# Performance work log

Hardware: AMD Instinct MI355X
Metric: run time of the kernel (lower is better)

The kernel has to match this reference:

```python
import jax, jax.numpy as jnp
import numpy as np

NUM_STEPS = 100
FRACTAL_STEPS = 1


def setup_inputs() -> dict:
    key = jax.random.key(0)
    B, D, NF = 16384, 256, 32  # batch, input_shape(==num_hidden), num_filters
    ks = jax.random.split(key, 6)

    def lin_w(k, fin, fout):
        return (jax.random.normal(k, (fin, fout), jnp.float32) / np.sqrt(fin)).astype(jnp.float32)

    return {
        "x": jax.random.normal(ks[0], (B, D), jnp.float32),
        "alpha": jnp.ones((D,), jnp.float32),
        "sigma": jnp.ones((D,), jnp.float32),
        "enc_w1": lin_w(ks[1], D, NF), "enc_b1": jnp.zeros((NF,), jnp.float32),
        "enc_w2": lin_w(ks[2], NF, D), "enc_b2": jnp.zeros((D,), jnp.float32),
        "gen_w1": lin_w(ks[3], D, NF), "gen_b1": jnp.zeros((NF,), jnp.float32),
        "gen_w2": lin_w(ks[4], NF, NF), "gen_b2": jnp.zeros((NF,), jnp.float32),
        "gen_w3": lin_w(ks[5], NF, D), "gen_b3": jnp.zeros((D,), jnp.float32),
    }


def reference(x, alpha, sigma, enc_w1, enc_b1, enc_w2, enc_b2,
              gen_w1, gen_b1, gen_w2, gen_b2, gen_w3, gen_b3):
    base_key = jax.random.key(42)
    D = x.shape[-1]

    def diffuse(z, i):
        # alpha_t = exp(-0.5*alpha*t/T), sigma_t = exp(0.5*sigma*t/T)
        t = i / NUM_STEPS
        a = jnp.exp(-0.5 * alpha * t)
        s = jnp.exp(0.5 * sigma * t)
        noise = jax.random.normal(jax.random.fold_in(base_key, i), z.shape, z.dtype)
        return z * a + s * noise

    # encoder: Linear -> ReLU -> Linear
    z = jnp.maximum(x @ enc_w1 + enc_b1, 0.0) @ enc_w2 + enc_b2  # [B, D]
    z = jnp.tile(z, (FRACTAL_STEPS, 1))

    def step(z, i):
        z = diffuse(z, i)
        h = jnp.maximum(z @ gen_w1 + gen_b1, 0.0)
        h = jnp.maximum(h @ gen_w2 + gen_b2, 0.0)
        z = jnp.maximum(h @ gen_w3 + gen_b3, 0.0)  # generator output then F.relu
        return z, None

    # loop i = T-1 .. 1 (diffuse + generator); the i == 0 iteration only diffuses
    ts = jnp.arange(NUM_STEPS - 1, 0, -1)
    z, _ = jax.lax.scan(step, z, ts)
    z = diffuse(z, jnp.int32(0))
    return z.reshape(-1, D)
```

## Files before the change

kernel.cpp:

```cpp
#include <hip/hip_runtime.h>
#include <stdint.h>


#define NUM_STEPS 100
#define HALFB 8192
#define THREADS 512
#define ZSTR 264
#define WS 36

#define Z_OFF   0
#define W1_OFF  (Z_OFF + 64*ZSTR)
#define W3_OFF  (W1_OFF + 256*32)
#define W2_OFF  (W3_OFF + 256*WS)
#define HB_OFF  (W2_OFF + 32*WS)
#define AE_OFF  (HB_OFF + 64*WS)
#define SE_OFF  (AE_OFF + 512)
#define B1_OFF  (SE_OFF + 512)
#define B2_OFF  (B1_OFF + 32)
#define B3_OFF  (B2_OFF + 32)
#define LDS_FLOATS (B3_OFF + 256)
#define LDS_BYTES  (LDS_FLOATS * 4)

static_assert(LDS_BYTES <= 160*1024, "LDS overflow");

typedef float v2f __attribute__((ext_vector_type(2)));
typedef float v4f __attribute__((ext_vector_type(4)));

#define PKFMA(acc,s0,s1)   asm("v_pk_fma_f32 %0, %1, %2, %0" : "+v"(acc) : "v"(s0), "v"(s1))
#define PKFMA_L(acc,s0,s1) asm("v_pk_fma_f32 %0, %1, %2, %0 op_sel:[0,0,0] op_sel_hi:[0,1,1]" : "+v"(acc) : "v"(s0), "v"(s1))
#define PKFMA_H(acc,s0,s1) asm("v_pk_fma_f32 %0, %1, %2, %0 op_sel:[1,0,0] op_sel_hi:[1,1,1]" : "+v"(acc) : "v"(s0), "v"(s1))
#define PKMUL(d,a,b)       asm("v_pk_mul_f32 %0, %1, %2" : "=v"(d) : "v"(a), "v"(b))

__device__ __forceinline__ uint32_t rotl32(uint32_t v, int n) {
  return (v << n) | (v >> (32 - n));
}

__device__ __forceinline__ void tf2x32(uint32_t k0, uint32_t k1,
                                       uint32_t& x0, uint32_t& x1) {
  uint32_t k2 = k0 ^ k1 ^ 0x1BD11BDAu;
  x0 += k0; x1 += k1;
#define TFR(r) { x0 += x1; x1 = rotl32(x1,(r)); x1 ^= x0; }
  TFR(13) TFR(15) TFR(26) TFR(6)
  x0 += k1; x1 += k2 + 1u;
  TFR(17) TFR(29) TFR(16) TFR(24)
  x0 += k2; x1 += k0 + 2u;
  TFR(13) TFR(15) TFR(26) TFR(6)
  x0 += k0; x1 += k1 + 3u;
  TFR(17) TFR(29) TFR(16) TFR(24)
  x0 += k1; x1 += k2 + 4u;
  TFR(13) TFR(15) TFR(26) TFR(6)
  x0 += k2; x1 += k0 + 5u;
#undef TFR
}

__device__ __forceinline__ uint32_t tf_bits(uint32_t k0, uint32_t k1, uint32_t n) {
  uint32_t x0 = 0u, x1 = n;
  tf2x32(k0, k1, x0, x1);
  return x0 ^ x1;
}

__device__ __forceinline__ v2f b2n_pk(uint32_t b0, uint32_t b1) {
  const float MN = -0.99999994039535522461f;
  v2f f = { __uint_as_float((b0 >> 9) | 0x3F800000u),
            __uint_as_float((b1 >> 9) | 0x3F800000u) };
  v2f fm = f - 1.0f;
  v2f u = __builtin_elementwise_fma(fm, (v2f)2.0f, (v2f)MN);
  u = __builtin_elementwise_max(u, (v2f)MN);
  v2f x2 = u * u;
  v2f om = 1.0f - x2;
  v2f w  = { -__logf(om.x), -__logf(om.y) };
  v2f ws = w - 2.5f;
  v2f ps = (v2f)2.81022636e-08f;
  ps = __builtin_elementwise_fma(ps, ws, (v2f)3.43273939e-07f);
  ps = __builtin_elementwise_fma(ps, ws, (v2f)-3.5233877e-06f);
  ps = __builtin_elementwise_fma(ps, ws, (v2f)-4.39150654e-06f);
  ps = __builtin_elementwise_fma(ps, ws, (v2f)0.00021858087f);
  ps = __builtin_elementwise_fma(ps, ws, (v2f)-0.00125372503f);
  ps = __builtin_elementwise_fma(ps, ws, (v2f)-0.00417768164f);
  ps = __builtin_elementwise_fma(ps, ws, (v2f)0.246640727f);
  ps = __builtin_elementwise_fma(ps, ws, (v2f)1.50140941f);
  v2f sq = { sqrtf(w.x), sqrtf(w.y) };
  v2f wb = sq - 3.0f;
  v2f pb = (v2f)-0.000200214257f;
  pb = __builtin_elementwise_fma(pb, wb, (v2f)0.000100950558f);
  pb = __builtin_elementwise_fma(pb, wb, (v2f)0.00134934322f);
  pb = __builtin_elementwise_fma(pb, wb, (v2f)-0.00367342844f);
  pb = __builtin_elementwise_fma(pb, wb, (v2f)0.00573950773f);
  pb = __builtin_elementwise_fma(pb, wb, (v2f)-0.0076224613f);
  pb = __builtin_elementwise_fma(pb, wb, (v2f)0.00943887047f);
  pb = __builtin_elementwise_fma(pb, wb, (v2f)1.00167406f);
  pb = __builtin_elementwise_fma(pb, wb, (v2f)2.83297682f);
  v2f p = { (w.x < 5.0f) ? ps.x : pb.x,
            (w.y < 5.0f) ? ps.y : pb.y };
  return (p * u) * 1.41421356237309515f;
}

__global__ __launch_bounds__(THREADS, 2)
void gdiff_kernel(const float* __restrict__ x,
                  const float* __restrict__ alpha, const float* __restrict__ sigma,
                  const float* __restrict__ ew1, const float* __restrict__ eb1,
                  const float* __restrict__ ew2, const float* __restrict__ eb2,
                  const float* __restrict__ gw1, const float* __restrict__ gb1,
                  const float* __restrict__ gw2, const float* __restrict__ gb2,
                  const float* __restrict__ gw3, const float* __restrict__ gb3,
                  float* __restrict__ out)
{
  extern __shared__ float sm[];
  const int t    = threadIdx.x;
  const int pr   = t >> 4;
  const int c    = t & 15;
  const int half = c >> 3;
  const int cf   = c & 7;
  const int rid  = pr + (half << 5);
  const int zrow = rid * ZSTR;
  const uint32_t rowg = (uint32_t)(blockIdx.x * 32 + pr) + (uint32_t)(half * HALFB);
  const uint32_t nb   = rowg * 256u + (uint32_t)cf;

  v4f hq0, hq1, hq2, hq3, hq4, hq5, hq6, hq7;

  auto stage_w1 = [&](const float* __restrict__ w) {
    const int r = t >> 1, hh = t & 1;
#pragma unroll
    for (int q = 0; q < 4; ++q)
      *(v4f*)&sm[W1_OFF + r * 32 + hh * 16 + 4 * q] =
          *(const v4f*)&w[r * 32 + hh * 16 + 4 * q];
  };
  auto stage_w3t = [&](const float* __restrict__ w) {
    const int g = t >> 4, dc = t & 15;
#pragma unroll
    for (int q = 0; q < 4; ++q) {
      const int d0 = dc * 16 + q * 4;
      v4f v = *(const v4f*)&w[g * 256 + d0];
      sm[W3_OFF + (d0 + 0) * WS + g] = v.x;
      sm[W3_OFF + (d0 + 1) * WS + g] = v.y;
      sm[W3_OFF + (d0 + 2) * WS + g] = v.z;
      sm[W3_OFF + (d0 + 3) * WS + g] = v.w;
    }
  };

  auto layer1 = [&](v2f& h01, v2f& h23) {
    v4f bv = *(const v4f*)&sm[B1_OFF + 4 * cf];
    h01 = bv.xy; h23 = bv.zw;
    const float* zr_ = &sm[Z_OFF + zrow];
    const float* wp  = &sm[W1_OFF + 4 * cf];
#pragma unroll 4
    for (int d0 = 0; d0 < 256; d0 += 4) {
      v4f z4 = *(const v4f*)&zr_[d0];
      v4f wa = *(const v4f*)&wp[(d0 + 0) * 32];
      v4f wb = *(const v4f*)&wp[(d0 + 1) * 32];
      v4f wc = *(const v4f*)&wp[(d0 + 2) * 32];
      v4f wd = *(const v4f*)&wp[(d0 + 3) * 32];
      PKFMA_L(h01, z4.xy, wa.xy); PKFMA_L(h23, z4.xy, wa.zw);
      PKFMA_H(h01, z4.xy, wb.xy); PKFMA_H(h23, z4.xy, wb.zw);
      PKFMA_L(h01, z4.zw, wc.xy); PKFMA_L(h23, z4.zw, wc.zw);
      PKFMA_H(h01, z4.zw, wd.xy); PKFMA_H(h23, z4.zw, wd.zw);
    }
  };
  auto hwrite = [&](v2f a, v2f b) {
    v4f hv; hv.xy = a; hv.zw = b;
    *(v4f*)&sm[HB_OFF + rid * WS + 4 * cf] = hv;
  };
  auto hload = [&]() {
    const float* hb = &sm[HB_OFF + rid * WS];
    hq0 = *(const v4f*)&hb[0];  hq1 = *(const v4f*)&hb[4];
    hq2 = *(const v4f*)&hb[8];  hq3 = *(const v4f*)&hb[12];
    hq4 = *(const v4f*)&hb[16]; hq5 = *(const v4f*)&hb[20];
    hq6 = *(const v4f*)&hb[24]; hq7 = *(const v4f*)&hb[28];
  };
  auto layer2 = [&](v2f& g01, v2f& g23) {
    v4f bv = *(const v4f*)&sm[B2_OFF + 4 * cf];
    g01 = bv.xy; g23 = bv.zw;
    const float* w2c = &sm[W2_OFF + 4 * cf];
#define L2M(hq, m) { \
    v4f wA = *(const v4f*)&w2c[(4*(m)+0)*WS]; \
    v4f wB = *(const v4f*)&w2c[(4*(m)+1)*WS]; \
    v4f wC = *(const v4f*)&w2c[(4*(m)+2)*WS]; \
    v4f wD = *(const v4f*)&w2c[(4*(m)+3)*WS]; \
    PKFMA_L(g01, hq.xy, wA.xy); PKFMA_L(g23, hq.xy, wA.zw); \
    PKFMA_H(g01, hq.xy, wB.xy); PKFMA_H(g23, hq.xy, wB.zw); \
    PKFMA_L(g01, hq.zw, wC.xy); PKFMA_L(g23, hq.zw, wC.zw); \
    PKFMA_H(g01, hq.zw, wD.xy); PKFMA_H(g23, hq.zw, wD.zw); }
    L2M(hq0,0) L2M(hq1,1) L2M(hq2,2) L2M(hq3,3)
    L2M(hq4,4) L2M(hq5,5) L2M(hq6,6) L2M(hq7,7)
#undef L2M
  };
  auto l3d = [&](uint32_t c0p, uint32_t c1p, const float* ae, const float* se, bool relu) {
    const float* w3b = &sm[W3_OFF];
#pragma unroll 2
    for (int kp = 0; kp < 16; ++kp) {
      const int dlo = cf + 16 * kp;
      const int dhi = dlo + 8;
      v2f acc0 = { sm[B3_OFF + dlo], 0.f };
      v2f acc1 = { sm[B3_OFF + dhi], 0.f };
      const float* wl = &w3b[dlo * WS];
      const float* wh = &w3b[dhi * WS];
#define L3M(hq, off) { \
      v4f wvl = *(const v4f*)&wl[off]; \
      v4f wvh = *(const v4f*)&wh[off]; \
      PKFMA(acc0, hq.xy, wvl.xy); PKFMA(acc0, hq.zw, wvl.zw); \
      PKFMA(acc1, hq.xy, wvh.xy); PKFMA(acc1, hq.zw, wvh.zw); }
      L3M(hq0, 0)  L3M(hq1, 4)  L3M(hq2, 8)  L3M(hq3, 12)
      L3M(hq4, 16) L3M(hq5, 20) L3M(hq6, 24) L3M(hq7, 28)
#undef L3M
      float z0 = acc0.x + acc0.y;
      float z1 = acc1.x + acc1.y;
      if (relu) { z0 = fmaxf(z0, 0.f); z1 = fmaxf(z1, 0.f); }
      const uint32_t n0 = nb + (uint32_t)(16 * kp);
      const uint32_t b0 = tf_bits(c0p, c1p, n0);
      const uint32_t b1 = tf_bits(c0p, c1p, n0 + 8u);
      v2f nrm = b2n_pk(b0, b1);
      v2f a2 = { ae[dlo], ae[dhi] };
      v2f s2 = { se[dlo], se[dhi] };
      v2f z2 = { z0, z1 };
      v2f zd; PKMUL(zd, z2, a2); PKFMA(zd, s2, nrm);
      sm[Z_OFF + zrow + dlo] = zd.x;
      sm[Z_OFF + zrow + dhi] = zd.y;
    }
  };

  {
    const int zr = t >> 3, jj = t & 7;
    const int gr = (zr < 32) ? (blockIdx.x * 32 + zr)
                             : (blockIdx.x * 32 + zr - 32 + HALFB);
    const v4f* src = (const v4f*)(x + (size_t)gr * 256 + jj * 32);
#pragma unroll
    for (int q = 0; q < 8; ++q)
      *(v4f*)&sm[Z_OFF + zr * ZSTR + jj * 32 + q * 4] = src[q];
  }
  stage_w1(ew1);
  stage_w3t(ew2);
  if (t < 256) sm[B3_OFF + t] = eb2[t];
  if (t < 32)  sm[B1_OFF + t] = eb1[t];
  {
    const float t99 = 99.0f / 100.0f;
    if (t < 256) sm[AE_OFF + 256 + t]       = __expf(-0.5f * alpha[t] * t99);
    else         sm[SE_OFF + 256 + (t-256)] = __expf( 0.5f * sigma[t-256] * t99);
  }
  __syncthreads();

  {
    v2f h01, h23;
    layer1(h01, h23);
    h01 = __builtin_elementwise_max(h01, (v2f)0.f);
    h23 = __builtin_elementwise_max(h23, (v2f)0.f);
    hwrite(h01, h23);
    hload();
    uint32_t e0 = 0u, e1 = 99u;
    tf2x32(0u, 42u, e0, e1);
    l3d(e0, e1, &sm[AE_OFF + 256], &sm[SE_OFF + 256], false);
  }
  __syncthreads();

  stage_w1(gw1);
  stage_w3t(gw3);
  if (t < 256) {
    sm[B3_OFF + t] = gb3[t];
    if (t < 32) { sm[B1_OFF + t] = gb1[t]; sm[B2_OFF + t] = gb2[t]; }
    const int r = t >> 3, s8 = t & 7;
    *(v4f*)&sm[W2_OFF + r * WS + 4 * s8] = *(const v4f*)&gw2[r * 32 + 4 * s8];
  }
  __syncthreads();

#pragma unroll 1
  for (int i = 99; i >= 1; --i) {
    const int j = i - 1;
    const float tt = (float)j / 100.0f;
    const int buf = (j & 1) << 8;
    if (t < 256) sm[AE_OFF + buf + t]       = __expf(-0.5f * alpha[t] * tt);
    else         sm[SE_OFF + buf + (t-256)] = __expf( 0.5f * sigma[t-256] * tt);
    __syncthreads();

    v2f h01, h23;
    layer1(h01, h23);
    h01 = __builtin_elementwise_max(h01, (v2f)0.f);
    h23 = __builtin_elementwise_max(h23, (v2f)0.f);
    hwrite(h01, h23);
    hload();

    v2f g01, g23;
    layer2(g01, g23);
    g01 = __builtin_elementwise_max(g01, (v2f)0.f);
    g23 = __builtin_elementwise_max(g23, (v2f)0.f);
    hwrite(g01, g23);
    hload();

    uint32_t e0 = 0u, e1 = (uint32_t)j;
    tf2x32(0u, 42u, e0, e1);
    l3d(e0, e1, &sm[AE_OFF + buf], &sm[SE_OFF + buf], true);
  }
  __syncthreads();

  {
    const int zr = t >> 3, jj = t & 7;
    const int gr = (zr < 32) ? (blockIdx.x * 32 + zr)
                             : (blockIdx.x * 32 + zr - 32 + HALFB);
    v4f* dst = (v4f*)(out + (size_t)gr * 256 + jj * 32);
#pragma unroll
    for (int q = 0; q < 8; ++q)
      dst[q] = *(const v4f*)&sm[Z_OFF + zr * ZSTR + jj * 32 + q * 4];
  }
}

extern "C" void kernel_launch(void* const* d_in, const int* in_sizes, int n_in,
                              void* d_out, int out_size, void* d_ws, size_t ws_size,
                              hipStream_t stream) {
  (void)in_sizes; (void)n_in; (void)d_ws; (void)ws_size; (void)out_size;
  const float* x     = (const float*)d_in[0];
  const float* alpha = (const float*)d_in[1];
  const float* sigma = (const float*)d_in[2];
  const float* ew1   = (const float*)d_in[3];
  const float* eb1   = (const float*)d_in[4];
  const float* ew2   = (const float*)d_in[5];
  const float* eb2   = (const float*)d_in[6];
  const float* gw1   = (const float*)d_in[7];
  const float* gb1   = (const float*)d_in[8];
  const float* gw2   = (const float*)d_in[9];
  const float* gb2   = (const float*)d_in[10];
  const float* gw3   = (const float*)d_in[11];
  const float* gb3   = (const float*)d_in[12];
  float* out = (float*)d_out;

  (void)hipFuncSetAttribute((const void*)gdiff_kernel,
                            hipFuncAttributeMaxDynamicSharedMemorySize, LDS_BYTES);

  gdiff_kernel<<<256, THREADS, LDS_BYTES, stream>>>(
      x, alpha, sigma, ew1, eb1, ew2, eb2, gw1, gb1, gw2, gb2, gw3, gb3, out);
}
```

Baseline: 3.220 ms.

## Double threads per block with split-K layers, register diffusion coefficients, and branchy RNG

Raises the block to 1024 threads and splits the layer-1 and layer-2 reductions across two thread halves, combining them with a cross-lane shuffle. Each thread now produces 16 output columns instead of 32 in layer 3. Diffusion coefficients move into registers and are updated each step by multiplying with precomputed per-step ratios, which removes the per-step exp and one barrier. The change also uses alignbit for rotates and skips the large-tail branch of the inverse-erf polynomial unless some lane needs it. The risks are higher register pressure under the 4-wave occupancy bound, drift from the repeated coefficient multiplication, and the hoisted half-row z offset in LDS.

```diff
diff --git a/kernel.cpp b/kernel.cpp
--- a/kernel.cpp
+++ b/kernel.cpp
@@ -2,20 +2,19 @@
 #include <stdint.h>
 
 
-#define NUM_STEPS 100
 #define HALFB 8192
-#define THREADS 512
+#define THREADS 1024
 #define ZSTR 264
 #define WS 36
 
 #define Z_OFF   0
-#define W1_OFF  (Z_OFF + 64*ZSTR)
-#define W3_OFF  (W1_OFF + 256*32)
-#define W2_OFF  (W3_OFF + 256*WS)
-#define HB_OFF  (W2_OFF + 32*WS)
-#define AE_OFF  (HB_OFF + 64*WS)
-#define SE_OFF  (AE_OFF + 512)
-#define B1_OFF  (SE_OFF + 512)
+#define W1_OFF  16896
+#define W3_OFF  (W1_OFF + 8192)
+#define W2_OFF  (W3_OFF + 9216)
+#define HB_OFF  (W2_OFF + 1152)
+#define IA_OFF  (HB_OFF + 64*WS)
+#define IS_OFF  (IA_OFF + 256)
+#define B1_OFF  (IS_OFF + 256)
 #define B2_OFF  (B1_OFF + 32)
 #define B3_OFF  (B2_OFF + 32)
 #define LDS_FLOATS (B3_OFF + 256)
@@ -32,7 +31,7 @@
 #define PKMUL(d,a,b)       asm("v_pk_mul_f32 %0, %1, %2" : "=v"(d) : "v"(a), "v"(b))
 
 __device__ __forceinline__ uint32_t rotl32(uint32_t v, int n) {
-  return (v << n) | (v >> (32 - n));
+  return __builtin_amdgcn_alignbit(v, v, (uint32_t)(32 - n));
 }
 
 __device__ __forceinline__ void tf2x32(uint32_t k0, uint32_t k1,
@@ -79,23 +78,27 @@
   ps = __builtin_elementwise_fma(ps, ws, (v2f)-0.00417768164f);
   ps = __builtin_elementwise_fma(ps, ws, (v2f)0.246640727f);
   ps = __builtin_elementwise_fma(ps, ws, (v2f)1.50140941f);
-  v2f sq = { sqrtf(w.x), sqrtf(w.y) };
-  v2f wb = sq - 3.0f;
-  v2f pb = (v2f)-0.000200214257f;
-  pb = __builtin_elementwise_fma(pb, wb, (v2f)0.000100950558f);
-  pb = __builtin_elementwise_fma(pb, wb, (v2f)0.00134934322f);
-  pb = __builtin_elementwise_fma(pb, wb, (v2f)-0.00367342844f);
-  pb = __builtin_elementwise_fma(pb, wb, (v2f)0.00573950773f);
-  pb = __builtin_elementwise_fma(pb, wb, (v2f)-0.0076224613f);
-  pb = __builtin_elementwise_fma(pb, wb, (v2f)0.00943887047f);
-  pb = __builtin_elementwise_fma(pb, wb, (v2f)1.00167406f);
-  pb = __builtin_elementwise_fma(pb, wb, (v2f)2.83297682f);
-  v2f p = { (w.x < 5.0f) ? ps.x : pb.x,
-            (w.y < 5.0f) ? ps.y : pb.y };
+  v2f p = ps;
+  const int big = (w.x >= 5.0f) | (w.y >= 5.0f);
+  if (__any(big)) {
+    v2f sq = { sqrtf(w.x), sqrtf(w.y) };
+    v2f wb = sq - 3.0f;
+    v2f pb = (v2f)-0.000200214257f;
+    pb = __builtin_elementwise_fma(pb, wb, (v2f)0.000100950558f);
+    pb = __builtin_elementwise_fma(pb, wb, (v2f)0.00134934322f);
+    pb = __builtin_elementwise_fma(pb, wb, (v2f)-0.00367342844f);
+    pb = __builtin_elementwise_fma(pb, wb, (v2f)0.00573950773f);
+    pb = __builtin_elementwise_fma(pb, wb, (v2f)-0.0076224613f);
+    pb = __builtin_elementwise_fma(pb, wb, (v2f)0.00943887047f);
+    pb = __builtin_elementwise_fma(pb, wb, (v2f)1.00167406f);
+    pb = __builtin_elementwise_fma(pb, wb, (v2f)2.83297682f);
+    p.x = (w.x < 5.0f) ? ps.x : pb.x;
+    p.y = (w.y < 5.0f) ? ps.y : pb.y;
+  }
   return (p * u) * 1.41421356237309515f;
 }
 
-__global__ __launch_bounds__(THREADS, 2)
+__global__ __launch_bounds__(THREADS, 4)
 void gdiff_kernel(const float* __restrict__ x,
                   const float* __restrict__ alpha, const float* __restrict__ sigma,
                   const float* __restrict__ ew1, const float* __restrict__ eb1,
@@ -107,29 +110,32 @@
 {
   extern __shared__ float sm[];
   const int t    = threadIdx.x;
-  const int pr   = t >> 4;
-  const int c    = t & 15;
-  const int half = c >> 3;
-  const int cf   = c & 7;
+  const int pr   = t >> 5;
+  const int c    = t & 31;
+  const int half = c >> 4;
+  const int cf   = c & 15;
+  const int q    = cf & 7;
+  const int dh   = cf >> 3;
   const int rid  = pr + (half << 5);
-  const int zrow = rid * ZSTR;
-  const uint32_t rowg = (uint32_t)(blockIdx.x * 32 + pr) + (uint32_t)(half * HALFB);
+  const int zrow = rid * ZSTR + (half << 3);
+  const uint32_t rowg = (uint32_t)(blockIdx.x * 32 + pr + half * HALFB);
   const uint32_t nb   = rowg * 256u + (uint32_t)cf;
 
   v4f hq0, hq1, hq2, hq3, hq4, hq5, hq6, hq7;
+  v2f av[8], sv[8];
 
   auto stage_w1 = [&](const float* __restrict__ w) {
-    const int r = t >> 1, hh = t & 1;
-#pragma unroll
-    for (int q = 0; q < 4; ++q)
-      *(v4f*)&sm[W1_OFF + r * 32 + hh * 16 + 4 * q] =
-          *(const v4f*)&w[r * 32 + hh * 16 + 4 * q];
+    const int r = t >> 2, part = t & 3;
+#pragma unroll
+    for (int s = 0; s < 2; ++s)
+      *(v4f*)&sm[W1_OFF + r * 32 + part * 8 + 4 * s] =
+          *(const v4f*)&w[r * 32 + part * 8 + 4 * s];
   };
   auto stage_w3t = [&](const float* __restrict__ w) {
-    const int g = t >> 4, dc = t & 15;
-#pragma unroll
-    for (int q = 0; q < 4; ++q) {
-      const int d0 = dc * 16 + q * 4;
+    const int g = t >> 5, dc = t & 31;
+#pragma unroll
+    for (int s = 0; s < 2; ++s) {
+      const int d0 = dc * 8 + s * 4;
       v4f v = *(const v4f*)&w[g * 256 + d0];
       sm[W3_OFF + (d0 + 0) * WS + g] = v.x;
       sm[W3_OFF + (d0 + 1) * WS + g] = v.y;
@@ -139,12 +145,13 @@
   };
 
   auto layer1 = [&](v2f& h01, v2f& h23) {
-    v4f bv = *(const v4f*)&sm[B1_OFF + 4 * cf];
+    v4f bv = { 0.f, 0.f, 0.f, 0.f };
+    if (!dh) bv = *(const v4f*)&sm[B1_OFF + 4 * q];
     h01 = bv.xy; h23 = bv.zw;
-    const float* zr_ = &sm[Z_OFF + zrow];
-    const float* wp  = &sm[W1_OFF + 4 * cf];
+    const float* zr_ = &sm[zrow + (dh << 7)];
+    const float* wp  = &sm[W1_OFF + (dh << 12) + 4 * q];
 #pragma unroll 4
-    for (int d0 = 0; d0 < 256; d0 += 4) {
+    for (int d0 = 0; d0 < 128; d0 += 4) {
       v4f z4 = *(const v4f*)&zr_[d0];
       v4f wa = *(const v4f*)&wp[(d0 + 0) * 32];
       v4f wb = *(const v4f*)&wp[(d0 + 1) * 32];
@@ -156,11 +163,17 @@
       PKFMA_H(h01, z4.zw, wd.xy); PKFMA_H(h23, z4.zw, wd.zw);
     }
   };
+  auto red8_relu = [&](v2f& a, v2f& b) {
+    a.x += __shfl_xor(a.x, 8); a.y += __shfl_xor(a.y, 8);
+    b.x += __shfl_xor(b.x, 8); b.y += __shfl_xor(b.y, 8);
+    a = __builtin_elementwise_max(a, (v2f)0.f);
+    b = __builtin_elementwise_max(b, (v2f)0.f);
+  };
   auto hwrite = [&](v2f a, v2f b) {
-    v4f hv; hv.xy = a; hv.zw = b;
-    *(v4f*)&sm[HB_OFF + rid * WS + 4 * cf] = hv;
-  };
-  auto hload = [&]() {
+    if (!dh) { v4f hv; hv.xy = a; hv.zw = b;
+               *(v4f*)&sm[HB_OFF + rid * WS + 4 * q] = hv; }
+  };
+  auto hload8 = [&]() {
     const float* hb = &sm[HB_OFF + rid * WS];
     hq0 = *(const v4f*)&hb[0];  hq1 = *(const v4f*)&hb[4];
     hq2 = *(const v4f*)&hb[8];  hq3 = *(const v4f*)&hb[12];
@@ -168,86 +181,87 @@
     hq6 = *(const v4f*)&hb[24]; hq7 = *(const v4f*)&hb[28];
   };
   auto layer2 = [&](v2f& g01, v2f& g23) {
-    v4f bv = *(const v4f*)&sm[B2_OFF + 4 * cf];
+    const float* hb = &sm[HB_OFF + rid * WS + (dh << 4)];
+    v4f hA = *(const v4f*)&hb[0], hB = *(const v4f*)&hb[4];
+    v4f hC = *(const v4f*)&hb[8], hD = *(const v4f*)&hb[12];
+    v4f bv = { 0.f, 0.f, 0.f, 0.f };
+    if (!dh) bv = *(const v4f*)&sm[B2_OFF + 4 * q];
     g01 = bv.xy; g23 = bv.zw;
-    const float* w2c = &sm[W2_OFF + 4 * cf];
-#define L2M(hq, m) { \
-    v4f wA = *(const v4f*)&w2c[(4*(m)+0)*WS]; \
-    v4f wB = *(const v4f*)&w2c[(4*(m)+1)*WS]; \
-    v4f wC = *(const v4f*)&w2c[(4*(m)+2)*WS]; \
-    v4f wD = *(const v4f*)&w2c[(4*(m)+3)*WS]; \
-    PKFMA_L(g01, hq.xy, wA.xy); PKFMA_L(g23, hq.xy, wA.zw); \
-    PKFMA_H(g01, hq.xy, wB.xy); PKFMA_H(g23, hq.xy, wB.zw); \
-    PKFMA_L(g01, hq.zw, wC.xy); PKFMA_L(g23, hq.zw, wC.zw); \
-    PKFMA_H(g01, hq.zw, wD.xy); PKFMA_H(g23, hq.zw, wD.zw); }
-    L2M(hq0,0) L2M(hq1,1) L2M(hq2,2) L2M(hq3,3)
-    L2M(hq4,4) L2M(hq5,5) L2M(hq6,6) L2M(hq7,7)
+    const float* w2c = &sm[W2_OFF + (dh << 4) * WS + 4 * q];
+#define L2M(hqm, mm) { \
+    v4f wA = *(const v4f*)&w2c[(4*(mm)+0)*WS]; \
+    v4f wB = *(const v4f*)&w2c[(4*(mm)+1)*WS]; \
+    v4f wC = *(const v4f*)&w2c[(4*(mm)+2)*WS]; \
+    v4f wD = *(const v4f*)&w2c[(4*(mm)+3)*WS]; \
+    PKFMA_L(g01, hqm.xy, wA.xy); PKFMA_L(g23, hqm.xy, wA.zw); \
+    PKFMA_H(g01, hqm.xy, wB.xy); PKFMA_H(g23, hqm.xy, wB.zw); \
+    PKFMA_L(g01, hqm.zw, wC.xy); PKFMA_L(g23, hqm.zw, wC.zw); \
+    PKFMA_H(g01, hqm.zw, wD.xy); PKFMA_H(g23, hqm.zw, wD.zw); }
+    L2M(hA,0) L2M(hB,1) L2M(hC,2) L2M(hD,3)
 #undef L2M
   };
-  auto l3d = [&](uint32_t c0p, uint32_t c1p, const float* ae, const float* se, bool relu) {
-    const float* w3b = &sm[W3_OFF];
-#pragma unroll 2
-    for (int kp = 0; kp < 16; ++kp) {
-      const int dlo = cf + 16 * kp;
-      const int dhi = dlo + 8;
+  auto l3d = [&](uint32_t e0, uint32_t e1, bool relu) {
+#pragma unroll
+    for (int kp = 0; kp < 8; ++kp) {
+      const int dlo = cf + 32 * kp;
+      const int dhi = dlo + 16;
       v2f acc0 = { sm[B3_OFF + dlo], 0.f };
       v2f acc1 = { sm[B3_OFF + dhi], 0.f };
-      const float* wl = &w3b[dlo * WS];
-      const float* wh = &w3b[dhi * WS];
-#define L3M(hq, off) { \
+      const float* wl = &sm[W3_OFF + dlo * WS];
+      const float* wh = &sm[W3_OFF + dhi * WS];
+#define L3M(hqm, off) { \
       v4f wvl = *(const v4f*)&wl[off]; \
       v4f wvh = *(const v4f*)&wh[off]; \
-      PKFMA(acc0, hq.xy, wvl.xy); PKFMA(acc0, hq.zw, wvl.zw); \
-      PKFMA(acc1, hq.xy, wvh.xy); PKFMA(acc1, hq.zw, wvh.zw); }
+      PKFMA(acc0, hqm.xy, wvl.xy); PKFMA(acc0, hqm.zw, wvl.zw); \
+      PKFMA(acc1, hqm.xy, wvh.xy); PKFMA(acc1, hqm.zw, wvh.zw); }
       L3M(hq0, 0)  L3M(hq1, 4)  L3M(hq2, 8)  L3M(hq3, 12)
       L3M(hq4, 16) L3M(hq5, 20) L3M(hq6, 24) L3M(hq7, 28)
 #undef L3M
       float z0 = acc0.x + acc0.y;
       float z1 = acc1.x + acc1.y;
       if (relu) { z0 = fmaxf(z0, 0.f); z1 = fmaxf(z1, 0.f); }
-      const uint32_t n0 = nb + (uint32_t)(16 * kp);
-      const uint32_t b0 = tf_bits(c0p, c1p, n0);
-      const uint32_t b1 = tf_bits(c0p, c1p, n0 + 8u);
-      v2f nrm = b2n_pk(b0, b1);
-      v2f a2 = { ae[dlo], ae[dhi] };
-      v2f s2 = { se[dlo], se[dhi] };
+      const uint32_t n0 = nb + (uint32_t)(32 * kp);
+      v2f nrm = b2n_pk(tf_bits(e0, e1, n0), tf_bits(e0, e1, n0 + 16u));
       v2f z2 = { z0, z1 };
-      v2f zd; PKMUL(zd, z2, a2); PKFMA(zd, s2, nrm);
-      sm[Z_OFF + zrow + dlo] = zd.x;
-      sm[Z_OFF + zrow + dhi] = zd.y;
+      v2f zd; PKMUL(zd, z2, av[kp]); PKFMA(zd, sv[kp], nrm);
+      sm[zrow + dlo] = zd.x;
+      sm[zrow + dhi] = zd.y;
     }
   };
 
   {
-    const int zr = t >> 3, jj = t & 7;
+    const int zr = t >> 4, jj = t & 15;
     const int gr = (zr < 32) ? (blockIdx.x * 32 + zr)
                              : (blockIdx.x * 32 + zr - 32 + HALFB);
-    const v4f* src = (const v4f*)(x + (size_t)gr * 256 + jj * 32);
-#pragma unroll
-    for (int q = 0; q < 8; ++q)
-      *(v4f*)&sm[Z_OFF + zr * ZSTR + jj * 32 + q * 4] = src[q];
+    const v4f* src = (const v4f*)(x + (size_t)gr * 256 + jj * 16);
+    const int zb = zr * ZSTR + ((zr >> 5) << 3);
+#pragma unroll
+    for (int s = 0; s < 4; ++s)
+      *(v4f*)&sm[zb + jj * 16 + 4 * s] = src[s];
   }
   stage_w1(ew1);
   stage_w3t(ew2);
+  if (t < 256)      sm[IA_OFF + t]         = __expf( 0.5f * alpha[t] * 0.01f);
+  else if (t < 512) sm[IS_OFF + (t - 256)] = __expf(-0.5f * sigma[t - 256] * 0.01f);
   if (t < 256) sm[B3_OFF + t] = eb2[t];
   if (t < 32)  sm[B1_OFF + t] = eb1[t];
-  {
-    const float t99 = 99.0f / 100.0f;
-    if (t < 256) sm[AE_OFF + 256 + t]       = __expf(-0.5f * alpha[t] * t99);
-    else         sm[SE_OFF + 256 + (t-256)] = __expf( 0.5f * sigma[t-256] * t99);
+#pragma unroll
+  for (int kp = 0; kp < 8; ++kp) {
+    const int dlo = cf + 32 * kp, dhi = dlo + 16;
+    av[kp] = v2f{ __expf(-0.5f * alpha[dlo] * 0.99f), __expf(-0.5f * alpha[dhi] * 0.99f) };
+    sv[kp] = v2f{ __expf( 0.5f * sigma[dlo] * 0.99f), __expf( 0.5f * sigma[dhi] * 0.99f) };
   }
   __syncthreads();
 
   {
     v2f h01, h23;
     layer1(h01, h23);
-    h01 = __builtin_elementwise_max(h01, (v2f)0.f);
-    h23 = __builtin_elementwise_max(h23, (v2f)0.f);
+    red8_relu(h01, h23);
     hwrite(h01, h23);
-    hload();
+    hload8();
     uint32_t e0 = 0u, e1 = 99u;
     tf2x32(0u, 42u, e0, e1);
-    l3d(e0, e1, &sm[AE_OFF + 256], &sm[SE_OFF + 256], false);
+    l3d(e0, e1, false);
   }
   __syncthreads();
 
@@ -264,40 +278,40 @@
 #pragma unroll 1
   for (int i = 99; i >= 1; --i) {
     const int j = i - 1;
-    const float tt = (float)j / 100.0f;
-    const int buf = (j & 1) << 8;
-    if (t < 256) sm[AE_OFF + buf + t]       = __expf(-0.5f * alpha[t] * tt);
-    else         sm[SE_OFF + buf + (t-256)] = __expf( 0.5f * sigma[t-256] * tt);
-    __syncthreads();
-
+#pragma unroll
+    for (int kp = 0; kp < 8; ++kp) {
+      const int dlo = cf + 32 * kp, dhi = dlo + 16;
+      v2f ia  = { sm[IA_OFF + dlo], sm[IA_OFF + dhi] };
+      v2f is_ = { sm[IS_OFF + dlo], sm[IS_OFF + dhi] };
+      PKMUL(av[kp], av[kp], ia);
+      PKMUL(sv[kp], sv[kp], is_);
+    }
     v2f h01, h23;
     layer1(h01, h23);
-    h01 = __builtin_elementwise_max(h01, (v2f)0.f);
-    h23 = __builtin_elementwise_max(h23, (v2f)0.f);
+    red8_relu(h01, h23);
     hwrite(h01, h23);
-    hload();
 
     v2f g01, g23;
     layer2(g01, g23);
-    g01 = __builtin_elementwise_max(g01, (v2f)0.f);
-    g23 = __builtin_elementwise_max(g23, (v2f)0.f);
+    red8_relu(g01, g23);
     hwrite(g01, g23);
-    hload();
+    hload8();
 
     uint32_t e0 = 0u, e1 = (uint32_t)j;
     tf2x32(0u, 42u, e0, e1);
-    l3d(e0, e1, &sm[AE_OFF + buf], &sm[SE_OFF + buf], true);
+    l3d(e0, e1, true);
   }
   __syncthreads();
 
   {
-    const int zr = t >> 3, jj = t & 7;
+    const int zr = t >> 4, jj = t & 15;
     const int gr = (zr < 32) ? (blockIdx.x * 32 + zr)
                              : (blockIdx.x * 32 + zr - 32 + HALFB);
-    v4f* dst = (v4f*)(out + (size_t)gr * 256 + jj * 32);
-#pragma unroll
-    for (int q = 0; q < 8; ++q)
-      dst[q] = *(const v4f*)&sm[Z_OFF + zr * ZSTR + jj * 32 + q * 4];
+    v4f* dst = (v4f*)(out + (size_t)gr * 256 + jj * 16);
+    const int zb = zr * ZSTR + ((zr >> 5) << 3);
+#pragma unroll
+    for (int s = 0; s < 4; ++s)
+      dst[s] = *(const v4f*)&sm[zb + jj * 16 + 4 * s];
   }
 }
 
```

Result: slower. 4.588 ms (+42.5%).
